# Optimization experiments

Hardware: AMD Instinct MI355X
Metric: run time of the kernel (lower is better)

## Reference

```python
import jax, jax.numpy as jnp
import numpy as np

K = 16          # per-chain hidden states: int(sqrt(args.hidden_dim=256))
K2 = K * K      # joint enumerated state (w, x)
SCALE = 1.0     # handlers.scale(scale=args.scale)


def setup_inputs() -> dict:
    key = jax.random.key(0)
    ks = jax.random.split(key, 8)
    N, T, D, B = 4096, 512, 88, 1024
    # Bernoulli observations (binary piano-roll style data)
    sequences = (jax.random.uniform(ks[0], (N, T, D)) < 0.3).astype(jnp.float32)
    lengths = jax.random.randint(ks[1], (N,), T // 4, T + 1).astype(jnp.int32)
    mb = jax.random.randint(ks[2], (B,), 0, N).astype(jnp.int32)
    mask = jnp.ones((B,), dtype=bool)

    def simplex(k, shape):
        p = jax.random.uniform(k, shape) + 0.1
        return p / p.sum(-1, keepdims=True)

    probs_w = simplex(ks[3], (K, K))
    probs_x = simplex(ks[4], (K, K))
    w_init = simplex(ks[5], (K,))
    x_init = simplex(ks[6], (K,))
    probs_y = jax.random.uniform(ks[7], (K, K, D), minval=0.05, maxval=0.95)
    return dict(sequences=sequences, probs_w=probs_w, probs_x=probs_x,
                w_init=w_init, x_init=x_init, probs_y=probs_y,
                lengths=lengths, mb=mb, mask=mask)


def reference(sequences, probs_w, probs_x, w_init, x_init, probs_y, lengths, mb, mask):
    """Exact marginal log-likelihood of the factorial HMM (what parallel
    enumeration over w_t, x_t computes): forward algorithm over the joint
    256-state chain with factorized transitions and Bernoulli emissions."""
    T = sequences.shape[1]
    seq = sequences[mb]          # [B, T, D]
    len_mb = lengths[mb]         # [B]

    # Bernoulli emission log-probs, contracted over tones plate (dim -1):
    # logB[t, b, k] = sum_d [ y*log(p) + (1-y)*log(1-p) ],  k = (w, x) flat
    logp = jnp.log(probs_y).reshape(K2, -1)       # [K2, D]
    log1mp = jnp.log1p(-probs_y).reshape(K2, -1)  # [K2, D]
    logB = jnp.einsum('btd,kd->tbk', seq, logp - log1mp) + log1mp.sum(-1)  # [T,B,K2]

    # Factorized joint transition: logT[(w,x),(w',x')] = log p(w'|w) + log p(x'|x)
    logT = (jnp.log(probs_w)[:, None, :, None] +
            jnp.log(probs_x)[None, :, None, :]).reshape(K2, K2)
    log_init = (jnp.log(w_init)[:, None] + jnp.log(x_init)[None, :]).reshape(K2)

    alpha0 = log_init + logB[0]  # [B, K2]; all lengths >= 1 here

    def step(alpha, inp):
        logb_t, t = inp
        nxt = jax.nn.logsumexp(alpha[:, :, None] + logT[None], axis=1) + logb_t
        valid = (t < len_mb)[:, None]            # mask: t < lengths[mb]
        return jnp.where(valid, nxt, alpha), None

    alpha, _ = jax.lax.scan(step, alpha0, (logB[1:], jnp.arange(1, T)))
    loglik = jax.nn.logsumexp(alpha, axis=-1)    # [B]
    return SCALE * jnp.sum(jnp.where(mask, loglik, 0.0))
```

## Files before the change

### kernel.cpp

```cpp
#include <hip/hip_runtime.h>


typedef _Float16 h4 __attribute__((ext_vector_type(4)));
typedef _Float16 h8 __attribute__((ext_vector_type(8)));
typedef float v4f __attribute__((ext_vector_type(4)));

#define TT 512
#define DD 88
#define NB 1024
#define LOG4096 8.317766167f

#define WS_BF   0ull
#define WS_BIAS 49152ull
#define WS_WF   (WS_BIAS + 1024ull)
#define WS_XF   (WS_WF + 512ull)

__device__ inline float dpp_wave_sum(float x) {
  union fi { float f; int i; };
  fi v; v.f = x;
#define DPPADD(ctrl, rmask)                                              \
  { fi t; t.i = __builtin_amdgcn_update_dpp(0, v.i, ctrl, rmask, 0xf, false); \
    v.f += t.f; }
  DPPADD(0x111, 0xf)
  DPPADD(0x112, 0xf)
  DPPADD(0x114, 0xf)
  DPPADD(0x118, 0xf)
  DPPADD(0x142, 0xa)
  DPPADD(0x143, 0xc)
#undef DPPADD
  fi o; o.i = __builtin_amdgcn_readlane(v.i, 63);
  return o.f;
}

__global__ __launch_bounds__(256) void prep_kernel(
    const float* __restrict__ pw, const float* __restrict__ px,
    const float* __restrict__ py, float* __restrict__ out,
    unsigned char* __restrict__ ws) {
  int tid = threadIdx.x;
  int blk = blockIdx.x;
  _Float16* bfrag = (_Float16*)(ws + WS_BF);
  float* bias = (float*)(ws + WS_BIAS);
  _Float16* wf = (_Float16*)(ws + WS_WF);
  _Float16* xf = (_Float16*)(ws + WS_XF);
  if (blk == 0) {
    float s = 0.f;
    for (int d = 0; d < DD; ++d) s += __logf(1.0f - py[tid * DD + d]);
    bias[tid] = s;
  } else if (blk == 1) {
    if (tid == 0) out[0] = 0.0f;
    if (tid < 64) {
      int q = tid >> 4, c = tid & 15;
      #pragma unroll
      for (int i = 0; i < 4; ++i) {
        wf[tid * 4 + i] = (_Float16)pw[(4 * q + i) * 16 + c];
        xf[tid * 4 + i] = (_Float16)px[(4 * q + i) * 16 + c];
      }
    }
  } else {
    int idx = (blk - 2) * 256 + tid;
    int j = idx & 7, l = (idx >> 3) & 63, n = (idx >> 9) & 15, c = idx >> 13;
    int state = n * 16 + (l & 15);
    int d = c * 32 + (l >> 4) * 8 + j;
    float v = 0.f;
    if (d < DD) {
      float p = py[state * DD + d];
      v = __logf(p) - __logf(1.0f - p);
    }
    bfrag[idx] = (_Float16)v;
  }
}

__global__ __launch_bounds__(64, 1) void fused_kernel(
    const float* __restrict__ seq, const int* __restrict__ lengths,
    const int* __restrict__ mb, const float* __restrict__ w_init,
    const float* __restrict__ x_init, float* __restrict__ out,
    const unsigned char* __restrict__ ws) {
  __shared__ _Float16 bt_s[16 * 264];
  __shared__ float m_s[16];
  int b = blockIdx.x, lane = threadIdx.x;
  int q = lane >> 4, cc = lane & 15;
  int item = mb[b], len = lengths[item];
  int nch = (len + 15) >> 4;

  union { uint2 u; h4 h; } wfu, xfu;
  wfu.u = *(const uint2*)((const _Float16*)(ws + WS_WF) + lane * 4);
  xfu.u = *(const uint2*)((const _Float16*)(ws + WS_XF) + lane * 4);
  h4 Wf = wfu.h, Xf = xfu.h;

  uint4 bf[48];
  const uint4* gbf = (const uint4*)(ws + WS_BF);
  #pragma unroll
  for (int i = 0; i < 48; ++i) bf[i] = gbf[i * 64 + lane];

  const float* bias = (const float*)(ws + WS_BIAS);
  float biasr[16];
  #pragma unroll
  for (int n = 0; n < 16; ++n) biasr[n] = bias[16 * n + cc];

  const float* sbase = seq + (size_t)item * TT * DD;

  float4 pf[6];
  {
    const float* srow = sbase + (size_t)cc * DD;
    #pragma unroll
    for (int ci = 0; ci < 3; ++ci) {
      int d0 = ci * 32 + q * 8;
      if (d0 < DD) {
        pf[2 * ci]     = *(const float4*)(srow + d0);
        pf[2 * ci + 1] = *(const float4*)(srow + d0 + 4);
      }
    }
  }

  h4 sv;
  sv[0] = (_Float16)0.f; sv[1] = (_Float16)0.f;
  sv[2] = (_Float16)0.f; sv[3] = (_Float16)0.f;
  float logacc = 0.f;
  int t = 0;
  bool done = false;
  int toff = cc * 16 + 4 * q;

  for (int c = 0; c < nch; ++c) {
    h8 af[3];
    #pragma unroll
    for (int ci = 0; ci < 3; ++ci) {
      h8 a;
      int d0 = ci * 32 + q * 8;
      if (d0 < DD) {
        float4 f0 = pf[2 * ci], f1 = pf[2 * ci + 1];
        a[0] = (_Float16)f0.x; a[1] = (_Float16)f0.y;
        a[2] = (_Float16)f0.z; a[3] = (_Float16)f0.w;
        a[4] = (_Float16)f1.x; a[5] = (_Float16)f1.y;
        a[6] = (_Float16)f1.z; a[7] = (_Float16)f1.w;
      } else {
        #pragma unroll
        for (int j = 0; j < 8; ++j) a[j] = (_Float16)0.f;
      }
      af[ci] = a;
    }
    {
      int cp = (c + 1 < nch) ? c + 1 : nch - 1;
      const float* srow = sbase + (size_t)(16 * cp + cc) * DD;
      #pragma unroll
      for (int ci = 0; ci < 3; ++ci) {
        int d0 = ci * 32 + q * 8;
        if (d0 < DD) {
          pf[2 * ci]     = *(const float4*)(srow + d0);
          pf[2 * ci + 1] = *(const float4*)(srow + d0 + 4);
        }
      }
    }
    v4f acc[16];
    #pragma unroll
    for (int n = 0; n < 16; ++n) {
      v4f a0 = (v4f){0.f, 0.f, 0.f, 0.f};
      #pragma unroll
      for (int ci = 0; ci < 3; ++ci) {
        union { uint4 u; h8 h; } bfh;
        bfh.u = bf[ci * 16 + n];
        a0 = __builtin_amdgcn_mfma_f32_16x16x32_f16(af[ci], bfh.h, a0, 0, 0, 0);
      }
      acc[n] = a0;
    }
    #pragma unroll
    for (int n = 0; n < 16; ++n) {
      float bn = biasr[n];
      acc[n][0] += bn; acc[n][1] += bn; acc[n][2] += bn; acc[n][3] += bn;
    }
    float mrow[4];
    #pragma unroll
    for (int r = 0; r < 4; ++r) {
      float mv = acc[0][r];
      #pragma unroll
      for (int n = 1; n < 16; ++n) mv = fmaxf(mv, acc[n][r]);
      mv = fmaxf(mv, __shfl_xor(mv, 1));
      mv = fmaxf(mv, __shfl_xor(mv, 2));
      mv = fmaxf(mv, __shfl_xor(mv, 4));
      mv = fmaxf(mv, __shfl_xor(mv, 8));
      mrow[r] = mv;
    }
    if (cc == 0) {
      #pragma unroll
      for (int r = 0; r < 4; ++r) m_s[4 * q + r] = mrow[r];
    }
    #pragma unroll
    for (int r = 0; r < 4; ++r) {
      union { _Float16 h[16]; uint4 u[2]; } pk;
      #pragma unroll
      for (int n = 0; n < 16; ++n)
        pk.h[n] = (_Float16)__expf(acc[n][r] - mrow[r]);
      _Float16* dst = bt_s + (4 * q + r) * 264 + cc * 16;
      *(uint4*)(dst) = pk.u[0];
      *(uint4*)(dst + 8) = pk.u[1];
    }

    if (c == 0) {
      union { uint2 u; h4 h; } bt0;
      bt0.u = *(const uint2*)(bt_s + toff);
      float xiv = x_init[cc] * 4096.0f;
      sv[0] = (_Float16)(w_init[4 * q + 0] * xiv * (float)bt0.h[0]);
      sv[1] = (_Float16)(w_init[4 * q + 1] * xiv * (float)bt0.h[1]);
      sv[2] = (_Float16)(w_init[4 * q + 2] * xiv * (float)bt0.h[2]);
      sv[3] = (_Float16)(w_init[4 * q + 3] * xiv * (float)bt0.h[3]);
      logacc = m_s[0] - LOG4096;
      t = 1;
      done = (len <= 1);
    }
    int i0 = (c == 0) ? 1 : 0;
    #pragma unroll
    for (int i2 = 0; i2 < 16; ++i2) {
      if (i2 >= i0 && !done) {
        if (t >= len) {
          done = true;
        } else {
          float rl = (float)sv[0] + (float)sv[1] +
                     (float)sv[2] + (float)sv[3];
          float Rn = dpp_wave_sum(rl);
          v4f zz = (v4f){0.f, 0.f, 0.f, 0.f};
          v4f d1 = __builtin_amdgcn_mfma_f32_16x16x16f16(sv, Wf, zz, 0, 0, 0);
          h4 a2;
          { auto lo = __builtin_amdgcn_cvt_pkrtz(d1[0], d1[1]);
            auto hi = __builtin_amdgcn_cvt_pkrtz(d1[2], d1[3]);
            a2[0] = lo[0]; a2[1] = lo[1]; a2[2] = hi[0]; a2[3] = hi[1]; }
          v4f d2 = __builtin_amdgcn_mfma_f32_16x16x16f16(a2, Xf, zz, 0, 0, 0);
          union { uint2 u; h4 h; } bt;
          bt.u = *(const uint2*)(bt_s + i2 * 264 + toff);
          h4 pm;
          { auto lo = __builtin_amdgcn_cvt_pkrtz(d2[0], d2[1]);
            auto hi = __builtin_amdgcn_cvt_pkrtz(d2[2], d2[3]);
            pm[0] = lo[0]; pm[1] = lo[1]; pm[2] = hi[0]; pm[3] = hi[1]; }
          pm = pm * bt.h;
          float fsc = __builtin_amdgcn_rcpf(Rn) * 4096.0f;
          _Float16 fh = (_Float16)fsc;
          h4 fv; fv[0] = fh; fv[1] = fh; fv[2] = fh; fv[3] = fh;
          sv = pm * fv;
          logacc += __logf(Rn) + m_s[i2] - LOG4096;
          ++t;
        }
      }
    }
  }

  float Sf = dpp_wave_sum((float)sv[0] + (float)sv[1] +
                          (float)sv[2] + (float)sv[3]);
  float ll = logacc + __logf(Sf);
  if (lane == 0) atomicAdd(out, ll);
}

extern "C" void kernel_launch(void* const* d_in, const int* in_sizes, int n_in,
                              void* d_out, int out_size, void* d_ws, size_t ws_size,
                              hipStream_t stream) {
  const float* seq = (const float*)d_in[0];
  const float* pw = (const float*)d_in[1];
  const float* px = (const float*)d_in[2];
  const float* wi = (const float*)d_in[3];
  const float* xi = (const float*)d_in[4];
  const float* py = (const float*)d_in[5];
  const int* lengths = (const int*)d_in[6];
  const int* mb = (const int*)d_in[7];
  float* out = (float*)d_out;
  unsigned char* ws = (unsigned char*)d_ws;

  prep_kernel<<<98, 256, 0, stream>>>(pw, px, py, out, ws);
  fused_kernel<<<NB, 64, 0, stream>>>(seq, lengths, mb, wi, xi, out, ws);
}
```

Before: 939.1 us.

## Split emission producer and recurrence consumer into separate waves with double-buffered LDS

The block grows to two waves. Wave 0 computes the emission log-probabilities for the next 16-step chunk with MFMA and writes them to a double-buffered shared array, while wave 1 runs the serial forward recurrence on the current chunk. The two waves hand off through __syncthreads once per chunk. To fit two waves per SIMD, one third of the B fragments move from registers to LDS, the bias is folded into the accumulator init, and the scale factor is applied to bt before the product. This is meant to hide the emission compute behind the latency-bound recurrence, at the cost of barrier overhead and extra LDS traffic.

Result: faster. 904.8 us (-3.7%).

```diff
diff --git a/kernel.cpp b/kernel.cpp
--- a/kernel.cpp
+++ b/kernel.cpp
@@ -70,181 +70,192 @@
   }
 }
 
-__global__ __launch_bounds__(64, 1) void fused_kernel(
+__global__ __launch_bounds__(128, 2) void fused_kernel(
     const float* __restrict__ seq, const int* __restrict__ lengths,
     const int* __restrict__ mb, const float* __restrict__ w_init,
     const float* __restrict__ x_init, float* __restrict__ out,
     const unsigned char* __restrict__ ws) {
-  __shared__ _Float16 bt_s[16 * 264];
-  __shared__ float m_s[16];
-  int b = blockIdx.x, lane = threadIdx.x;
+  __shared__ _Float16 bt_s[2][16 * 264];
+  __shared__ float m_s[2][16];
+  __shared__ uint4 bfl[16 * 64];
+  int b = blockIdx.x;
+  int tid = threadIdx.x;
+  int wv = tid >> 6, lane = tid & 63;
   int q = lane >> 4, cc = lane & 15;
   int item = mb[b], len = lengths[item];
   int nch = (len + 15) >> 4;
 
-  union { uint2 u; h4 h; } wfu, xfu;
-  wfu.u = *(const uint2*)((const _Float16*)(ws + WS_WF) + lane * 4);
-  xfu.u = *(const uint2*)((const _Float16*)(ws + WS_XF) + lane * 4);
-  h4 Wf = wfu.h, Xf = xfu.h;
-
-  uint4 bf[48];
-  const uint4* gbf = (const uint4*)(ws + WS_BF);
-  #pragma unroll
-  for (int i = 0; i < 48; ++i) bf[i] = gbf[i * 64 + lane];
-
-  const float* bias = (const float*)(ws + WS_BIAS);
-  float biasr[16];
-  #pragma unroll
-  for (int n = 0; n < 16; ++n) biasr[n] = bias[16 * n + cc];
-
-  const float* sbase = seq + (size_t)item * TT * DD;
-
-  float4 pf[6];
-  {
-    const float* srow = sbase + (size_t)cc * DD;
-    #pragma unroll
-    for (int ci = 0; ci < 3; ++ci) {
-      int d0 = ci * 32 + q * 8;
-      if (d0 < DD) {
-        pf[2 * ci]     = *(const float4*)(srow + d0);
-        pf[2 * ci + 1] = *(const float4*)(srow + d0 + 4);
-      }
-    }
-  }
-
-  h4 sv;
-  sv[0] = (_Float16)0.f; sv[1] = (_Float16)0.f;
-  sv[2] = (_Float16)0.f; sv[3] = (_Float16)0.f;
-  float logacc = 0.f;
-  int t = 0;
-  bool done = false;
-  int toff = cc * 16 + 4 * q;
-
-  for (int c = 0; c < nch; ++c) {
-    h8 af[3];
-    #pragma unroll
-    for (int ci = 0; ci < 3; ++ci) {
-      h8 a;
-      int d0 = ci * 32 + q * 8;
-      if (d0 < DD) {
-        float4 f0 = pf[2 * ci], f1 = pf[2 * ci + 1];
-        a[0] = (_Float16)f0.x; a[1] = (_Float16)f0.y;
-        a[2] = (_Float16)f0.z; a[3] = (_Float16)f0.w;
-        a[4] = (_Float16)f1.x; a[5] = (_Float16)f1.y;
-        a[6] = (_Float16)f1.z; a[7] = (_Float16)f1.w;
-      } else {
-        #pragma unroll
-        for (int j = 0; j < 8; ++j) a[j] = (_Float16)0.f;
-      }
-      af[ci] = a;
-    }
+  if (wv == 0) {
+    const uint4* gbf = (const uint4*)(ws + WS_BF);
+    uint4 bfv[32];
+    #pragma unroll
+    for (int i = 0; i < 32; ++i) bfv[i] = gbf[i * 64 + lane];
+    #pragma unroll
+    for (int i = 0; i < 16; ++i) bfl[i * 64 + lane] = gbf[(32 + i) * 64 + lane];
+    const float* bias = (const float*)(ws + WS_BIAS);
+    float biasr[16];
+    #pragma unroll
+    for (int n = 0; n < 16; ++n) biasr[n] = bias[16 * n + cc];
+    const float* sbase = seq + (size_t)item * TT * DD;
+    float4 pf[6];
     {
-      int cp = (c + 1 < nch) ? c + 1 : nch - 1;
-      const float* srow = sbase + (size_t)(16 * cp + cc) * DD;
+      const float* srow = sbase + (size_t)cc * DD;
       #pragma unroll
       for (int ci = 0; ci < 3; ++ci) {
         int d0 = ci * 32 + q * 8;
         if (d0 < DD) {
-          pf[2 * ci]     = *(const float4*)(srow + d0);
+          pf[2 * ci] = *(const float4*)(srow + d0);
           pf[2 * ci + 1] = *(const float4*)(srow + d0 + 4);
         }
       }
     }
-    v4f acc[16];
-    #pragma unroll
-    for (int n = 0; n < 16; ++n) {
-      v4f a0 = (v4f){0.f, 0.f, 0.f, 0.f};
+#define PRODUCE(cp, bi)                                                  \
+    {                                                                    \
+      h8 af[3];                                                          \
+      _Pragma("unroll") for (int ci = 0; ci < 3; ++ci) {                 \
+        h8 a;                                                            \
+        int d0 = ci * 32 + q * 8;                                        \
+        if (d0 < DD) {                                                   \
+          float4 f0 = pf[2 * ci], f1 = pf[2 * ci + 1];                   \
+          a[0] = (_Float16)f0.x; a[1] = (_Float16)f0.y;                  \
+          a[2] = (_Float16)f0.z; a[3] = (_Float16)f0.w;                  \
+          a[4] = (_Float16)f1.x; a[5] = (_Float16)f1.y;                  \
+          a[6] = (_Float16)f1.z; a[7] = (_Float16)f1.w;                  \
+        } else {                                                         \
+          _Pragma("unroll") for (int j = 0; j < 8; ++j)                  \
+            a[j] = (_Float16)0.f;                                        \
+        }                                                                \
+        af[ci] = a;                                                      \
+      }                                                                  \
+      {                                                                  \
+        int cnx = (cp) + 1 < nch ? (cp) + 1 : nch - 1;                   \
+        const float* srow = sbase + (size_t)(16 * cnx + cc) * DD;        \
+        _Pragma("unroll") for (int ci = 0; ci < 3; ++ci) {               \
+          int d0 = ci * 32 + q * 8;                                      \
+          if (d0 < DD) {                                                 \
+            pf[2 * ci] = *(const float4*)(srow + d0);                    \
+            pf[2 * ci + 1] = *(const float4*)(srow + d0 + 4);            \
+          }                                                              \
+        }                                                                \
+      }                                                                  \
+      v4f acc[16];                                                       \
+      _Pragma("unroll") for (int n = 0; n < 16; ++n) {                   \
+        float bn = biasr[n];                                             \
+        acc[n] = (v4f){bn, bn, bn, bn};                                  \
+      }                                                                  \
+      _Pragma("unroll") for (int n = 0; n < 16; ++n) {                   \
+        union { uint4 u; h8 h; } b0, b1, b2;                             \
+        b0.u = bfv[n]; b1.u = bfv[16 + n];                               \
+        b2.u = bfl[n * 64 + lane];                                       \
+        acc[n] = __builtin_amdgcn_mfma_f32_16x16x32_f16(af[0], b0.h, acc[n], 0, 0, 0); \
+        acc[n] = __builtin_amdgcn_mfma_f32_16x16x32_f16(af[1], b1.h, acc[n], 0, 0, 0); \
+        acc[n] = __builtin_amdgcn_mfma_f32_16x16x32_f16(af[2], b2.h, acc[n], 0, 0, 0); \
+      }                                                                  \
+      float mrow[4];                                                     \
+      _Pragma("unroll") for (int r = 0; r < 4; ++r) {                    \
+        float mv = acc[0][r];                                            \
+        _Pragma("unroll") for (int n = 1; n < 16; ++n)                   \
+          mv = fmaxf(mv, acc[n][r]);                                     \
+        mv = fmaxf(mv, __shfl_xor(mv, 1));                               \
+        mv = fmaxf(mv, __shfl_xor(mv, 2));                               \
+        mv = fmaxf(mv, __shfl_xor(mv, 4));                               \
+        mv = fmaxf(mv, __shfl_xor(mv, 8));                               \
+        mrow[r] = mv;                                                    \
+      }                                                                  \
+      if (cc == 0) {                                                     \
+        _Pragma("unroll") for (int r = 0; r < 4; ++r)                    \
+          m_s[bi][4 * q + r] = mrow[r];                                  \
+      }                                                                  \
+      _Pragma("unroll") for (int r = 0; r < 4; ++r) {                    \
+        union { _Float16 h[16]; uint4 u[2]; } pk;                        \
+        _Pragma("unroll") for (int n = 0; n < 16; ++n)                   \
+          pk.h[n] = (_Float16)__expf(acc[n][r] - mrow[r]);               \
+        _Float16* dst = bt_s[bi] + (4 * q + r) * 264 + cc * 16;          \
+        *(uint4*)dst = pk.u[0];                                          \
+        *(uint4*)(dst + 8) = pk.u[1];                                    \
+      }                                                                  \
+    }
+    PRODUCE(0, 0)
+    __syncthreads();
+    for (int c = 0; c < nch; ++c) {
+      if (c + 1 < nch) {
+        int bi = (c + 1) & 1;
+        PRODUCE(c + 1, bi)
+      }
+      __syncthreads();
+    }
+#undef PRODUCE
+  } else {
+    union { uint2 u; h4 h; } wfu, xfu;
+    wfu.u = *(const uint2*)((const _Float16*)(ws + WS_WF) + lane * 4);
+    xfu.u = *(const uint2*)((const _Float16*)(ws + WS_XF) + lane * 4);
+    h4 Wf = wfu.h, Xf = xfu.h;
+    float wir[4];
+    #pragma unroll
+    for (int r = 0; r < 4; ++r) wir[r] = w_init[4 * q + r];
+    float xiv = x_init[cc] * 4096.0f;
+    int toff = cc * 16 + 4 * q;
+    h4 sv;
+    sv[0] = (_Float16)0.f; sv[1] = (_Float16)0.f;
+    sv[2] = (_Float16)0.f; sv[3] = (_Float16)0.f;
+    float logacc = 0.f;
+    int t = 0;
+    bool done = false;
+    __syncthreads();
+    for (int c = 0; c < nch; ++c) {
+      const _Float16* bts = bt_s[c & 1];
+      const float* ms = m_s[c & 1];
+      if (c == 0) {
+        union { uint2 u; h4 h; } bt0;
+        bt0.u = *(const uint2*)(bts + toff);
+        sv[0] = (_Float16)(wir[0] * xiv * (float)bt0.h[0]);
+        sv[1] = (_Float16)(wir[1] * xiv * (float)bt0.h[1]);
+        sv[2] = (_Float16)(wir[2] * xiv * (float)bt0.h[2]);
+        sv[3] = (_Float16)(wir[3] * xiv * (float)bt0.h[3]);
+        logacc = ms[0] - LOG4096;
+        t = 1;
+        done = (len <= 1);
+      }
+      int i0 = (c == 0) ? 1 : 0;
       #pragma unroll
-      for (int ci = 0; ci < 3; ++ci) {
-        union { uint4 u; h8 h; } bfh;
-        bfh.u = bf[ci * 16 + n];
-        a0 = __builtin_amdgcn_mfma_f32_16x16x32_f16(af[ci], bfh.h, a0, 0, 0, 0);
-      }
-      acc[n] = a0;
-    }
-    #pragma unroll
-    for (int n = 0; n < 16; ++n) {
-      float bn = biasr[n];
-      acc[n][0] += bn; acc[n][1] += bn; acc[n][2] += bn; acc[n][3] += bn;
-    }
-    float mrow[4];
-    #pragma unroll
-    for (int r = 0; r < 4; ++r) {
-      float mv = acc[0][r];
-      #pragma unroll
-      for (int n = 1; n < 16; ++n) mv = fmaxf(mv, acc[n][r]);
-      mv = fmaxf(mv, __shfl_xor(mv, 1));
-      mv = fmaxf(mv, __shfl_xor(mv, 2));
-      mv = fmaxf(mv, __shfl_xor(mv, 4));
-      mv = fmaxf(mv, __shfl_xor(mv, 8));
-      mrow[r] = mv;
-    }
-    if (cc == 0) {
-      #pragma unroll
-      for (int r = 0; r < 4; ++r) m_s[4 * q + r] = mrow[r];
-    }
-    #pragma unroll
-    for (int r = 0; r < 4; ++r) {
-      union { _Float16 h[16]; uint4 u[2]; } pk;
-      #pragma unroll
-      for (int n = 0; n < 16; ++n)
-        pk.h[n] = (_Float16)__expf(acc[n][r] - mrow[r]);
-      _Float16* dst = bt_s + (4 * q + r) * 264 + cc * 16;
-      *(uint4*)(dst) = pk.u[0];
-      *(uint4*)(dst + 8) = pk.u[1];
-    }
-
-    if (c == 0) {
-      union { uint2 u; h4 h; } bt0;
-      bt0.u = *(const uint2*)(bt_s + toff);
-      float xiv = x_init[cc] * 4096.0f;
-      sv[0] = (_Float16)(w_init[4 * q + 0] * xiv * (float)bt0.h[0]);
-      sv[1] = (_Float16)(w_init[4 * q + 1] * xiv * (float)bt0.h[1]);
-      sv[2] = (_Float16)(w_init[4 * q + 2] * xiv * (float)bt0.h[2]);
-      sv[3] = (_Float16)(w_init[4 * q + 3] * xiv * (float)bt0.h[3]);
-      logacc = m_s[0] - LOG4096;
-      t = 1;
-      done = (len <= 1);
-    }
-    int i0 = (c == 0) ? 1 : 0;
-    #pragma unroll
-    for (int i2 = 0; i2 < 16; ++i2) {
-      if (i2 >= i0 && !done) {
-        if (t >= len) {
-          done = true;
-        } else {
-          float rl = (float)sv[0] + (float)sv[1] +
-                     (float)sv[2] + (float)sv[3];
-          float Rn = dpp_wave_sum(rl);
-          v4f zz = (v4f){0.f, 0.f, 0.f, 0.f};
-          v4f d1 = __builtin_amdgcn_mfma_f32_16x16x16f16(sv, Wf, zz, 0, 0, 0);
-          h4 a2;
-          { auto lo = __builtin_amdgcn_cvt_pkrtz(d1[0], d1[1]);
-            auto hi = __builtin_amdgcn_cvt_pkrtz(d1[2], d1[3]);
-            a2[0] = lo[0]; a2[1] = lo[1]; a2[2] = hi[0]; a2[3] = hi[1]; }
-          v4f d2 = __builtin_amdgcn_mfma_f32_16x16x16f16(a2, Xf, zz, 0, 0, 0);
-          union { uint2 u; h4 h; } bt;
-          bt.u = *(const uint2*)(bt_s + i2 * 264 + toff);
-          h4 pm;
-          { auto lo = __builtin_amdgcn_cvt_pkrtz(d2[0], d2[1]);
-            auto hi = __builtin_amdgcn_cvt_pkrtz(d2[2], d2[3]);
-            pm[0] = lo[0]; pm[1] = lo[1]; pm[2] = hi[0]; pm[3] = hi[1]; }
-          pm = pm * bt.h;
-          float fsc = __builtin_amdgcn_rcpf(Rn) * 4096.0f;
-          _Float16 fh = (_Float16)fsc;
-          h4 fv; fv[0] = fh; fv[1] = fh; fv[2] = fh; fv[3] = fh;
-          sv = pm * fv;
-          logacc += __logf(Rn) + m_s[i2] - LOG4096;
-          ++t;
+      for (int i2 = 0; i2 < 16; ++i2) {
+        if (i2 >= i0 && !done) {
+          if (t >= len) {
+            done = true;
+          } else {
+            float rl = (float)sv[0] + (float)sv[1] +
+                       (float)sv[2] + (float)sv[3];
+            float Rn = dpp_wave_sum(rl);
+            v4f zz = (v4f){0.f, 0.f, 0.f, 0.f};
+            v4f d1 = __builtin_amdgcn_mfma_f32_16x16x16f16(sv, Wf, zz, 0, 0, 0);
+            h4 a2;
+            { auto lo = __builtin_amdgcn_cvt_pkrtz(d1[0], d1[1]);
+              auto hi = __builtin_amdgcn_cvt_pkrtz(d1[2], d1[3]);
+              a2[0] = lo[0]; a2[1] = lo[1]; a2[2] = hi[0]; a2[3] = hi[1]; }
+            v4f d2 = __builtin_amdgcn_mfma_f32_16x16x16f16(a2, Xf, zz, 0, 0, 0);
+            union { uint2 u; h4 h; } bt;
+            bt.u = *(const uint2*)(bts + i2 * 264 + toff);
+            float fsc = __builtin_amdgcn_rcpf(Rn) * 4096.0f;
+            _Float16 fh = (_Float16)fsc;
+            h4 fv; fv[0] = fh; fv[1] = fh; fv[2] = fh; fv[3] = fh;
+            h4 btf = bt.h * fv;
+            h4 pm;
+            { auto lo = __builtin_amdgcn_cvt_pkrtz(d2[0], d2[1]);
+              auto hi = __builtin_amdgcn_cvt_pkrtz(d2[2], d2[3]);
+              pm[0] = lo[0]; pm[1] = lo[1]; pm[2] = hi[0]; pm[3] = hi[1]; }
+            sv = pm * btf;
+            logacc += __logf(Rn) + ms[i2] - LOG4096;
+            ++t;
+          }
         }
       }
-    }
+      __syncthreads();
+    }
+    float Sf = dpp_wave_sum((float)sv[0] + (float)sv[1] +
+                            (float)sv[2] + (float)sv[3]);
+    float ll = logacc + __logf(Sf);
+    if (lane == 0) atomicAdd(out, ll);
   }
-
-  float Sf = dpp_wave_sum((float)sv[0] + (float)sv[1] +
-                          (float)sv[2] + (float)sv[3]);
-  float ll = logacc + __logf(Sf);
-  if (lane == 0) atomicAdd(out, ll);
 }
 
 extern "C" void kernel_launch(void* const* d_in, const int* in_sizes, int n_in,
@@ -262,5 +273,5 @@
   unsigned char* ws = (unsigned char*)d_ws;
 
   prep_kernel<<<98, 256, 0, stream>>>(pw, px, py, out, ws);
-  fused_kernel<<<NB, 64, 0, stream>>>(seq, lengths, mb, wi, xi, out, ws);
-}
+  fused_kernel<<<NB, 128, 0, stream>>>(seq, lengths, mb, wi, xi, out, ws);
+}
```
